# Optimization experiments

Hardware: AMD Instinct MI355X
Metric: run time of the kernel (lower is better)

The kernel has to match this reference:

```python
import jax, jax.numpy as jnp
import numpy as np

IN_C = 128
MID_C = 128
EPS = 1e-5


def layer_norm(x, g, b):
    mu = jnp.mean(x, axis=-1, keepdims=True)
    var = jnp.mean(jnp.square(x - mu), axis=-1, keepdims=True)
    return (x - mu) * jax.lax.rsqrt(var + EPS) * g + b


def setup_inputs() -> dict:
    key = jax.random.key(0)
    ks = jax.random.split(key, 16)
    B, N = 1, 384
    s_in = 1.0 / np.sqrt(IN_C)
    s_mid = 1.0 / np.sqrt(MID_C)
    return {
        "x2d": jax.random.normal(ks[0], (B, N, N, IN_C), dtype=jnp.float32),
        "n1_g": jnp.ones((IN_C,), jnp.float32),
        "n1_b": jnp.zeros((IN_C,), jnp.float32),
        "n2_g": jnp.ones((MID_C,), jnp.float32),
        "n2_b": jnp.zeros((MID_C,), jnp.float32),
        "w1i": jax.random.uniform(ks[1], (MID_C, IN_C), jnp.float32, -s_in, s_in),
        "b1i": jnp.zeros((MID_C,), jnp.float32),
        "w1j": jax.random.uniform(ks[2], (MID_C, IN_C), jnp.float32, -s_in, s_in),
        "b1j": jnp.zeros((MID_C,), jnp.float32),
        "w1i_s": jax.random.uniform(ks[3], (MID_C, IN_C), jnp.float32, -s_in, s_in),
        "b1i_s": jnp.zeros((MID_C,), jnp.float32),
        "w1j_s": jax.random.uniform(ks[4], (MID_C, IN_C), jnp.float32, -s_in, s_in),
        "b1j_s": jnp.zeros((MID_C,), jnp.float32),
        "w2": jax.random.uniform(ks[5], (IN_C, MID_C), jnp.float32, -s_mid, s_mid),
        "b2": jnp.zeros((IN_C,), jnp.float32),
        "w3": jax.random.uniform(ks[6], (IN_C, IN_C), jnp.float32, -s_in, s_in),
        "b3": jnp.zeros((IN_C,), jnp.float32),
    }


def reference(x2d, n1_g, n1_b, n2_g, n2_b, w1i, b1i, w1j, b1j,
              w1i_s, b1i_s, w1j_s, b1j_s, w2, b2, w3, b3):
    # x2d: [B, N, N, C]
    x = layer_norm(x2d, n1_g, n1_b)
    i = (x @ w1i.T + b1i) * jax.nn.sigmoid(x @ w1i_s.T + b1i_s)  # [B,N,N,mid]
    j = (x @ w1j.T + b1j) * jax.nn.sigmoid(x @ w1j_s.T + b1j_s)  # [B,N,N,mid]
    out = jnp.einsum('bikc,bjkc->bijc', i, j)                    # contract over k
    out = layer_norm(out, n2_g, n2_b)
    out = out @ w2.T + b2
    out = out * jax.nn.sigmoid(x @ w3.T + b3)
    return out
```

## Files before the change

### kernel.cpp

```cpp
#include <hip/hip_runtime.h>

#define NN 384
#define CC 128
#define NPOS (NN * NN)

typedef short bf8_t __attribute__((ext_vector_type(8)));
typedef float f32x4_t __attribute__((ext_vector_type(4)));

#define MFMA16(a, b, c) __builtin_amdgcn_mfma_f32_16x16x32_bf16((a), (b), (c), 0, 0, 0)

__device__ __forceinline__ unsigned short f2bf(float f) {
  unsigned int u = __builtin_bit_cast(unsigned int, f);
  u += 0x7fffu + ((u >> 16) & 1u);
  return (unsigned short)(u >> 16);
}
__device__ __forceinline__ float bf2f(unsigned short s) {
  return __builtin_bit_cast(float, ((unsigned int)s) << 16);
}
__device__ __forceinline__ float sigm(float x) { return 1.0f / (1.0f + __expf(-x)); }

__global__ __launch_bounds__(256) void kW(const float* __restrict__ a,
                                          const float* __restrict__ b,
                                          const float* __restrict__ c,
                                          const float* __restrict__ d,
                                          const float* __restrict__ e,
                                          const float* __restrict__ f,
                                          unsigned short* __restrict__ o) {
  int idx = (blockIdx.x * 256 + threadIdx.x) * 4;
  const float* s = f;
  if (idx < 16384) s = a;
  else if (idx < 32768) s = b;
  else if (idx < 49152) s = c;
  else if (idx < 65536) s = d;
  else if (idx < 81920) s = e;
  int off = idx & 16383;
  float4 v = *(const float4*)(s + off);
  o[idx + 0] = f2bf(v.x);
  o[idx + 1] = f2bf(v.y);
  o[idx + 2] = f2bf(v.z);
  o[idx + 3] = f2bf(v.w);
}

__global__ __launch_bounds__(256, 2) void kA(
    const float* __restrict__ x, const float* __restrict__ n1g,
    const float* __restrict__ n1b, const unsigned short* __restrict__ wcat,
    const float* __restrict__ b1i, const float* __restrict__ b1is,
    const float* __restrict__ b1j, const float* __restrict__ b1js,
    const float* __restrict__ b3v, unsigned short* __restrict__ i_s,
    unsigned short* __restrict__ j_s, unsigned short* __restrict__ g3) {
  __shared__ __align__(16) unsigned short lds[17664];
  float* bl = (float*)(lds + 16384);

  int blk = blockIdx.x;
  int ii = blk / 3;
  int k0 = (blk % 3) * 128;
  int t = threadIdx.x;
  int lane = t & 63, wave = t >> 6;
  int lr = lane & 15, lh = lane >> 4;

  if (t < 160) {
    int m = t >> 5, e4 = t & 31;
    const float* bp = (m == 0) ? b1i : (m == 1) ? b1is : (m == 2) ? b1j : (m == 3) ? b1js : b3v;
    ((float4*)bl)[m * 32 + e4] = ((const float4*)bp)[e4];
  }

  {
    int pos = t >> 1, half = t & 1;
    const float* xr = x + (size_t)(ii * NN + k0 + pos) * CC + half * 64;
    float v[64];
    float s = 0.f;
#pragma unroll
    for (int a = 0; a < 16; ++a) {
      float4 f4 = ((const float4*)xr)[a];
      v[4 * a + 0] = f4.x; v[4 * a + 1] = f4.y;
      v[4 * a + 2] = f4.z; v[4 * a + 3] = f4.w;
      s += f4.x + f4.y + f4.z + f4.w;
    }
    s += __shfl_xor(s, 1);
    float mu = s * (1.0f / CC);
    float vs = 0.f;
#pragma unroll
    for (int a = 0; a < 64; ++a) { float d = v[a] - mu; vs += d * d; }
    vs += __shfl_xor(vs, 1);
    float rs = rsqrtf(vs * (1.0f / CC) + 1e-5f);
#pragma unroll
    for (int a8 = 0; a8 < 8; ++a8) {
      union { bf8_t v8; unsigned short e[8]; } u;
#pragma unroll
      for (int e = 0; e < 8; ++e) {
        int c = half * 64 + a8 * 8 + e;
        u.e[e] = f2bf((v[a8 * 8 + e] - mu) * rs * n1g[c] + n1b[c]);
      }
      int slot = (half * 8 + a8) ^ (pos & 7);
      *(bf8_t*)&lds[pos * 128 + slot * 8] = u.v8;
    }
  }
  __syncthreads();

  bf8_t xf[2][4];
#pragma unroll
  for (int nt = 0; nt < 2; ++nt)
#pragma unroll
    for (int kk = 0; kk < 4; ++kk) {
      int row = wave * 32 + nt * 16 + lr;
      int slot = (kk * 4 + lh) ^ (row & 7);
      xf[nt][kk] = *(const bf8_t*)&lds[row * 128 + slot * 8];
    }
  __syncthreads();

  constexpr int blk64[10] = {0, 2, 1, 3, 4, 6, 5, 7, 8, 9};
  auto ISSUE = [&](int k, int bsel) {
    const unsigned short* base = wcat + (size_t)blk64[k] * 8192;
#pragma unroll
    for (int it = 0; it < 4; ++it) {
      int u = it * 256 + t;
      int row = u >> 4, sl = u & 15;
      int slg = sl ^ (row & 7);
      __builtin_amdgcn_global_load_lds(
          (const __attribute__((address_space(1))) unsigned int*)(base + row * CC + slg * 8),
          (__attribute__((address_space(3))) unsigned int*)(lds + bsel * 8192 + u * 8), 16, 0, 0);
    }
  };
  auto COMP = [&](f32x4_t (&A)[4][2], const unsigned short* buf) {
#pragma unroll
    for (int ct = 0; ct < 4; ++ct)
#pragma unroll
      for (int kk = 0; kk < 4; ++kk) {
        int rv = ct * 16 + lr;
        int slot = (kk * 4 + lh) ^ (rv & 7);
        bf8_t w = *(const bf8_t*)&buf[rv * 128 + slot * 8];
#pragma unroll
        for (int nt = 0; nt < 2; ++nt) A[ct][nt] = MFMA16(w, xf[nt][kk], A[ct][nt]);
      }
  };

  f32x4_t z4 = {0.f, 0.f, 0.f, 0.f};
  f32x4_t accV[4][2], accG[4][2], acc3[2][4];
  ISSUE(0, 0);
#pragma unroll 10
  for (int k = 0; k < 10; ++k) {
    if (k == 2 || k == 4 || k == 6 || k == 8 || k == 9)
      asm volatile("s_waitcnt vmcnt(4)" ::: "memory");
    else
      asm volatile("s_waitcnt vmcnt(0)" ::: "memory");
    __builtin_amdgcn_s_barrier();
    __builtin_amdgcn_sched_barrier(0);
    if (k < 9) ISSUE(k + 1, (k + 1) & 1);
    unsigned short* buf = lds + (k & 1) * 8192;
    if (k < 8) {
      if ((k & 1) == 0) {
#pragma unroll
        for (int ct = 0; ct < 4; ++ct)
#pragma unroll
          for (int nt = 0; nt < 2; ++nt) accV[ct][nt] = z4;
        COMP(accV, buf);
      } else {
#pragma unroll
        for (int ct = 0; ct < 4; ++ct)
#pragma unroll
          for (int nt = 0; nt < 2; ++nt) accG[ct][nt] = z4;
        COMP(accG, buf);
        asm volatile("s_waitcnt lgkmcnt(0)" ::: "memory");
        __builtin_amdgcn_s_barrier();
        __builtin_amdgcn_sched_barrier(0);
        int pair = k >> 2, h = (k >> 1) & 1;
#pragma unroll
        for (int ct = 0; ct < 4; ++ct)
#pragma unroll
          for (int nt = 0; nt < 2; ++nt)
#pragma unroll
            for (int r = 0; r < 4; ++r) {
              int cl = ct * 16 + lh * 4 + r;
              int c = h * 64 + cl;
              float val = accV[ct][nt][r] + bl[pair * 256 + c];
              float gat = accG[ct][nt][r] + bl[pair * 256 + 128 + c];
              int pos = wave * 32 + nt * 16 + lr;
              int sw = ((ct * 4 + lh) & 7) << 4;
              buf[cl * 128 + (pos ^ sw)] = f2bf(val * sigm(gat));
            }
        asm volatile("s_waitcnt lgkmcnt(0)" ::: "memory");
        __builtin_amdgcn_s_barrier();
        __builtin_amdgcn_sched_barrier(0);
        unsigned short* dstm = pair ? j_s : i_s;
#pragma unroll
        for (int it = 0; it < 4; ++it) {
          int g = it * 256 + t;
          int cl = g >> 4, ch = g & 15;
          int s = (cl >> 2) & 7;
          bf8_t v = *(const bf8_t*)&buf[cl * 128 + ((ch ^ (s << 1)) * 8)];
          *(bf8_t*)(dstm + ((size_t)(h * 64 + cl) * NN + ii) * NN + k0 + ch * 8) = v;
        }
      }
    } else {
      int h = k - 8;
#pragma unroll
      for (int mt = 0; mt < 2; ++mt)
#pragma unroll
        for (int ct = 0; ct < 4; ++ct) acc3[mt][ct] = z4;
#pragma unroll
      for (int ct = 0; ct < 4; ++ct)
#pragma unroll
        for (int kk = 0; kk < 4; ++kk) {
          int rv = ct * 16 + lr;
          int slot = (kk * 4 + lh) ^ (rv & 7);
          bf8_t w = *(const bf8_t*)&buf[rv * 128 + slot * 8];
#pragma unroll
          for (int mt = 0; mt < 2; ++mt) acc3[mt][ct] = MFMA16(xf[mt][kk], w, acc3[mt][ct]);
        }
      asm volatile("s_waitcnt lgkmcnt(0)" ::: "memory");
      __builtin_amdgcn_s_barrier();
      __builtin_amdgcn_sched_barrier(0);
#pragma unroll
      for (int mt = 0; mt < 2; ++mt)
#pragma unroll
        for (int ct = 0; ct < 4; ++ct)
#pragma unroll
          for (int r = 0; r < 4; ++r) {
            int cl = ct * 16 + lr;
            int pos = wave * 32 + mt * 16 + lh * 4 + r;
            float gv = sigm(acc3[mt][ct][r] + bl[512 + h * 64 + cl]);
            int s2 = (pos >> 2) & 3;
            buf[pos * 64 + (cl ^ (s2 << 4))] = f2bf(gv);
          }
      asm volatile("s_waitcnt lgkmcnt(0)" ::: "memory");
      __builtin_amdgcn_s_barrier();
      __builtin_amdgcn_sched_barrier(0);
#pragma unroll
      for (int it = 0; it < 4; ++it) {
        int g = it * 256 + t;
        int p2 = g >> 3, cc2 = g & 7;
        int s2 = (p2 >> 2) & 3;
        bf8_t v = *(const bf8_t*)&buf[p2 * 64 + ((cc2 ^ (s2 << 1)) * 8)];
        *(bf8_t*)(g3 + (size_t)(ii * NN + k0 + p2) * CC + h * 64 + cc2 * 8) = v;
      }
    }
  }
}

__global__ __launch_bounds__(256) void kB(const unsigned short* __restrict__ i_s,
                                          const unsigned short* __restrict__ j_s,
                                          float* __restrict__ out_pre) {
  __shared__ unsigned short At[128][32];
  __shared__ unsigned short Bt[128][32];
  int b = blockIdx.x;
  int logical = (b & 7) * 144 + (b >> 3);
  int c = logical / 9;
  int tt = logical % 9;
  int i0 = (tt / 3) * 128, j0 = (tt % 3) * 128;
  const unsigned short* Ab = i_s + ((size_t)c * NN + i0) * NN;
  const unsigned short* Bb = j_s + ((size_t)c * NN + j0) * NN;
  int t = threadIdx.x, lane = t & 63, wave = t >> 6;
  int wi = (wave >> 1) * 64, wj = (wave & 1) * 64;
  int lr = lane & 15, lh = lane >> 4;
  int rsub = lane >> 2;
  int ksub = (lane & 3) * 8;

  f32x4_t z4 = {0.f, 0.f, 0.f, 0.f};
  f32x4_t acc[4][4];
#pragma unroll
  for (int mt = 0; mt < 4; ++mt)
#pragma unroll
    for (int nt = 0; nt < 4; ++nt) acc[mt][nt] = z4;

  for (int k0 = 0; k0 < NN; k0 += 32) {
#pragma unroll
    for (int half = 0; half < 2; ++half) {
      int r = half * 64 + wave * 16;
      __builtin_amdgcn_global_load_lds(
          (const __attribute__((address_space(1))) unsigned int*)(Ab + (size_t)(r + rsub) * NN + k0 + ksub),
          (__attribute__((address_space(3))) unsigned int*)&At[r][0], 16, 0, 0);
      __builtin_amdgcn_global_load_lds(
          (const __attribute__((address_space(1))) unsigned int*)(Bb + (size_t)(r + rsub) * NN + k0 + ksub),
          (__attribute__((address_space(3))) unsigned int*)&Bt[r][0], 16, 0, 0);
    }
    __syncthreads();
    bf8_t af2[4], bf2[4];
#pragma unroll
    for (int mt = 0; mt < 4; ++mt) af2[mt] = *(const bf8_t*)&At[wi + mt * 16 + lr][lh * 8];
#pragma unroll
    for (int nt = 0; nt < 4; ++nt) bf2[nt] = *(const bf8_t*)&Bt[wj + nt * 16 + lr][lh * 8];
#pragma unroll
    for (int mt = 0; mt < 4; ++mt)
#pragma unroll
      for (int nt = 0; nt < 4; ++nt) acc[mt][nt] = MFMA16(af2[mt], bf2[nt], acc[mt][nt]);
    __syncthreads();
  }
  float* orow = out_pre + ((size_t)c * NN + (i0 + wi)) * NN + (j0 + wj);
#pragma unroll
  for (int mt = 0; mt < 4; ++mt)
#pragma unroll
    for (int nt = 0; nt < 4; ++nt)
#pragma unroll
      for (int r = 0; r < 4; ++r)
        orow[(size_t)(mt * 16 + lh * 4 + r) * NN + nt * 16 + lr] = acc[mt][nt][r];
}

__global__ __launch_bounds__(256) void kC(const float* __restrict__ out_pre,
                                          const float* __restrict__ n2g,
                                          const float* __restrict__ n2b,
                                          const unsigned short* __restrict__ w2bf,
                                          const float* __restrict__ b2,
                                          const unsigned short* __restrict__ g3,
                                          float* __restrict__ out) {
  __shared__ unsigned short xs2[128][136];
  int b = blockIdx.x;
  int ii = b / 3, j0 = (b % 3) * 128;
  int t = threadIdx.x, lane = t & 63, wave = t >> 6;
  {
    int pos = t >> 1, half = t & 1;
    const float* src = out_pre + (size_t)half * 64 * NPOS + (size_t)ii * NN + j0 + pos;
    float v[64];
    float s = 0.f;
#pragma unroll
    for (int a2 = 0; a2 < 64; ++a2) { v[a2] = src[(size_t)a2 * NPOS]; s += v[a2]; }
    s += __shfl_xor(s, 1);
    float mu = s * (1.0f / CC);
    float vs = 0.f;
#pragma unroll
    for (int a2 = 0; a2 < 64; ++a2) { float d = v[a2] - mu; vs += d * d; }
    vs += __shfl_xor(vs, 1);
    float rs = rsqrtf(vs * (1.0f / CC) + 1e-5f);
#pragma unroll
    for (int a8 = 0; a8 < 8; ++a8) {
      union { bf8_t v8; unsigned short e[8]; } u;
#pragma unroll
      for (int e2 = 0; e2 < 8; ++e2) {
        int c = half * 64 + a8 * 8 + e2;
        u.e[e2] = f2bf((v[a8 * 8 + e2] - mu) * rs * n2g[c] + n2b[c]);
      }
      *(bf8_t*)&xs2[pos][half * 64 + a8 * 8] = u.v8;
    }
  }
  __syncthreads();
  int lr = lane & 15, lh = lane >> 4;
  bf8_t af2[2][4];
#pragma unroll
  for (int mt = 0; mt < 2; ++mt)
#pragma unroll
    for (int kk = 0; kk < 4; ++kk)
      af2[mt][kk] = *(const bf8_t*)&xs2[wave * 32 + mt * 16 + lr][kk * 32 + lh * 8];
  f32x4_t z4 = {0.f, 0.f, 0.f, 0.f};
  f32x4_t acc[2][8];
#pragma unroll
  for (int mt = 0; mt < 2; ++mt)
#pragma unroll
    for (int nt = 0; nt < 8; ++nt) acc[mt][nt] = z4;
#pragma unroll
  for (int nt = 0; nt < 8; ++nt) {
#pragma unroll
    for (int kk = 0; kk < 4; ++kk) {
      bf8_t bw = *(const bf8_t*)(w2bf + (size_t)(nt * 16 + lr) * CC + kk * 32 + lh * 8);
#pragma unroll
      for (int mt = 0; mt < 2; ++mt) acc[mt][nt] = MFMA16(af2[mt][kk], bw, acc[mt][nt]);
    }
  }
#pragma unroll
  for (int mt = 0; mt < 2; ++mt)
#pragma unroll
    for (int nt = 0; nt < 8; ++nt)
#pragma unroll
      for (int r = 0; r < 4; ++r) {
        int posl = wave * 32 + mt * 16 + lh * 4 + r;
        int c = nt * 16 + lr;
        size_t p = (size_t)ii * NN + j0 + posl;
        float y = acc[mt][nt][r] + b2[c];
        out[p * CC + c] = y * bf2f(g3[p * CC + c]);
      }
}

extern "C" void kernel_launch(void* const* d_in, const int* in_sizes, int n_in,
                              void* d_out, int out_size, void* d_ws, size_t ws_size,
                              hipStream_t stream) {
  (void)in_sizes; (void)n_in; (void)out_size; (void)ws_size;
  const float* x2d  = (const float*)d_in[0];
  const float* n1g  = (const float*)d_in[1];
  const float* n1b  = (const float*)d_in[2];
  const float* n2g  = (const float*)d_in[3];
  const float* n2b  = (const float*)d_in[4];
  const float* w1i  = (const float*)d_in[5];
  const float* b1i  = (const float*)d_in[6];
  const float* w1j  = (const float*)d_in[7];
  const float* b1j  = (const float*)d_in[8];
  const float* w1is = (const float*)d_in[9];
  const float* b1is = (const float*)d_in[10];
  const float* w1js = (const float*)d_in[11];
  const float* b1js = (const float*)d_in[12];
  const float* w2   = (const float*)d_in[13];
  const float* b2   = (const float*)d_in[14];
  const float* w3   = (const float*)d_in[15];
  const float* b3   = (const float*)d_in[16];

  char* ws = (char*)d_ws;
  unsigned short* wcat = (unsigned short*)ws;
  size_t TELEMS = (size_t)CC * NN * NN;
  unsigned short* i_s = (unsigned short*)(ws + 262144);
  unsigned short* j_s = i_s + TELEMS;
  unsigned short* g3  = j_s + TELEMS;
  float* out_pre = (float*)(ws + 262144 + 3 * TELEMS * 2);
  float* outp = (float*)d_out;

  kW<<<96, 256, 0, stream>>>(w1i, w1is, w1j, w1js, w3, w2, wcat);
  kA<<<1152, 256, 0, stream>>>(x2d, n1g, n1b, wcat, b1i, b1is, b1j, b1js, b3, i_s, j_s, g3);
  kB<<<1152, 256, 0, stream>>>(i_s, j_s, out_pre);
  kC<<<1152, 256, 0, stream>>>(out_pre, n2g, n2b, wcat + 5 * CC * CC, b2, g3, outp);
}
```

Baseline: 178.7 us.

## Write i/j projections position-major and transpose in a separate kernel

The projection kernel now writes the gated i/j outputs in natural position-major layout. It reuses one epilogue path for both the i/j pairs and the w3 gate. A new kT kernel stages 256-position tiles in LDS and transposes them to channel-major for the triangular contraction kernel. The aim is wider, simpler stores in kA and a single unified epilogue, at the cost of an extra full read and write of both i and j tensors plus a kernel launch. out_pre now aliases the i_nat/j_nat region to save workspace.

```diff
diff --git a/kernel.cpp b/kernel.cpp
--- a/kernel.cpp
+++ b/kernel.cpp
@@ -5,6 +5,7 @@
 #define NPOS (NN * NN)
 
 typedef short bf8_t __attribute__((ext_vector_type(8)));
+typedef short s4_t __attribute__((ext_vector_type(4)));
 typedef float f32x4_t __attribute__((ext_vector_type(4)));
 
 #define MFMA16(a, b, c) __builtin_amdgcn_mfma_f32_16x16x32_bf16((a), (b), (c), 0, 0, 0)
@@ -46,14 +47,15 @@
     const float* __restrict__ n1b, const unsigned short* __restrict__ wcat,
     const float* __restrict__ b1i, const float* __restrict__ b1is,
     const float* __restrict__ b1j, const float* __restrict__ b1js,
-    const float* __restrict__ b3v, unsigned short* __restrict__ i_s,
-    unsigned short* __restrict__ j_s, unsigned short* __restrict__ g3) {
+    const float* __restrict__ b3v, unsigned short* __restrict__ i_nat,
+    unsigned short* __restrict__ j_nat, unsigned short* __restrict__ g3) {
   __shared__ __align__(16) unsigned short lds[17664];
   float* bl = (float*)(lds + 16384);
 
   int blk = blockIdx.x;
   int ii = blk / 3;
   int k0 = (blk % 3) * 128;
+  int p0 = ii * NN + k0;
   int t = threadIdx.x;
   int lane = t & 63, wave = t >> 6;
   int lr = lane & 15, lh = lane >> 4;
@@ -66,7 +68,7 @@
 
   {
     int pos = t >> 1, half = t & 1;
-    const float* xr = x + (size_t)(ii * NN + k0 + pos) * CC + half * 64;
+    const float* xr = x + (size_t)(p0 + pos) * CC + half * 64;
     float v[64];
     float s = 0.f;
 #pragma unroll
@@ -121,7 +123,7 @@
           (__attribute__((address_space(3))) unsigned int*)(lds + bsel * 8192 + u * 8), 16, 0, 0);
     }
   };
-  auto COMP = [&](f32x4_t (&A)[4][2], const unsigned short* buf) {
+  auto COMP = [&](f32x4_t (&A)[2][4], const unsigned short* buf) {
 #pragma unroll
     for (int ct = 0; ct < 4; ++ct)
 #pragma unroll
@@ -130,12 +132,12 @@
         int slot = (kk * 4 + lh) ^ (rv & 7);
         bf8_t w = *(const bf8_t*)&buf[rv * 128 + slot * 8];
 #pragma unroll
-        for (int nt = 0; nt < 2; ++nt) A[ct][nt] = MFMA16(w, xf[nt][kk], A[ct][nt]);
+        for (int nt = 0; nt < 2; ++nt) A[nt][ct] = MFMA16(xf[nt][kk], w, A[nt][ct]);
       }
   };
 
   f32x4_t z4 = {0.f, 0.f, 0.f, 0.f};
-  f32x4_t accV[4][2], accG[4][2], acc3[2][4];
+  f32x4_t accV[2][4], accG[2][4];
   ISSUE(0, 0);
 #pragma unroll 10
   for (int k = 0; k < 10; ++k) {
@@ -147,93 +149,96 @@
     __builtin_amdgcn_sched_barrier(0);
     if (k < 9) ISSUE(k + 1, (k + 1) & 1);
     unsigned short* buf = lds + (k & 1) * 8192;
-    if (k < 8) {
-      if ((k & 1) == 0) {
-#pragma unroll
-        for (int ct = 0; ct < 4; ++ct)
-#pragma unroll
-          for (int nt = 0; nt < 2; ++nt) accV[ct][nt] = z4;
-        COMP(accV, buf);
-      } else {
-#pragma unroll
-        for (int ct = 0; ct < 4; ++ct)
-#pragma unroll
-          for (int nt = 0; nt < 2; ++nt) accG[ct][nt] = z4;
-        COMP(accG, buf);
-        asm volatile("s_waitcnt lgkmcnt(0)" ::: "memory");
-        __builtin_amdgcn_s_barrier();
-        __builtin_amdgcn_sched_barrier(0);
-        int pair = k >> 2, h = (k >> 1) & 1;
-#pragma unroll
-        for (int ct = 0; ct < 4; ++ct)
-#pragma unroll
-          for (int nt = 0; nt < 2; ++nt)
-#pragma unroll
-            for (int r = 0; r < 4; ++r) {
-              int cl = ct * 16 + lh * 4 + r;
-              int c = h * 64 + cl;
-              float val = accV[ct][nt][r] + bl[pair * 256 + c];
-              float gat = accG[ct][nt][r] + bl[pair * 256 + 128 + c];
-              int pos = wave * 32 + nt * 16 + lr;
-              int sw = ((ct * 4 + lh) & 7) << 4;
-              buf[cl * 128 + (pos ^ sw)] = f2bf(val * sigm(gat));
-            }
-        asm volatile("s_waitcnt lgkmcnt(0)" ::: "memory");
-        __builtin_amdgcn_s_barrier();
-        __builtin_amdgcn_sched_barrier(0);
-        unsigned short* dstm = pair ? j_s : i_s;
-#pragma unroll
-        for (int it = 0; it < 4; ++it) {
-          int g = it * 256 + t;
-          int cl = g >> 4, ch = g & 15;
-          int s = (cl >> 2) & 7;
-          bf8_t v = *(const bf8_t*)&buf[cl * 128 + ((ch ^ (s << 1)) * 8)];
-          *(bf8_t*)(dstm + ((size_t)(h * 64 + cl) * NN + ii) * NN + k0 + ch * 8) = v;
-        }
-      }
+    bool isPairV = (k < 8) && ((k & 1) == 0);
+    if (isPairV) {
+#pragma unroll
+      for (int nt = 0; nt < 2; ++nt)
+#pragma unroll
+        for (int ct = 0; ct < 4; ++ct) accV[nt][ct] = z4;
+      COMP(accV, buf);
     } else {
-      int h = k - 8;
-#pragma unroll
-      for (int mt = 0; mt < 2; ++mt)
-#pragma unroll
-        for (int ct = 0; ct < 4; ++ct) acc3[mt][ct] = z4;
-#pragma unroll
-      for (int ct = 0; ct < 4; ++ct)
-#pragma unroll
-        for (int kk = 0; kk < 4; ++kk) {
-          int rv = ct * 16 + lr;
-          int slot = (kk * 4 + lh) ^ (rv & 7);
-          bf8_t w = *(const bf8_t*)&buf[rv * 128 + slot * 8];
-#pragma unroll
-          for (int mt = 0; mt < 2; ++mt) acc3[mt][ct] = MFMA16(xf[mt][kk], w, acc3[mt][ct]);
-        }
+#pragma unroll
+      for (int nt = 0; nt < 2; ++nt)
+#pragma unroll
+        for (int ct = 0; ct < 4; ++ct) accG[nt][ct] = z4;
+      COMP(accG, buf);
       asm volatile("s_waitcnt lgkmcnt(0)" ::: "memory");
       __builtin_amdgcn_s_barrier();
       __builtin_amdgcn_sched_barrier(0);
-#pragma unroll
-      for (int mt = 0; mt < 2; ++mt)
+      int pair = k >> 2;
+      int h = (k < 8) ? ((k >> 1) & 1) : (k - 8);
+      unsigned short* dstm = (k >= 8) ? g3 : (pair ? j_nat : i_nat);
+#pragma unroll
+      for (int nt = 0; nt < 2; ++nt)
 #pragma unroll
         for (int ct = 0; ct < 4; ++ct)
 #pragma unroll
           for (int r = 0; r < 4; ++r) {
+            int pos = wave * 32 + nt * 16 + lh * 4 + r;
             int cl = ct * 16 + lr;
-            int pos = wave * 32 + mt * 16 + lh * 4 + r;
-            float gv = sigm(acc3[mt][ct][r] + bl[512 + h * 64 + cl]);
-            int s2 = (pos >> 2) & 3;
-            buf[pos * 64 + (cl ^ (s2 << 4))] = f2bf(gv);
+            float o;
+            if (k < 8) {
+              float val = accV[nt][ct][r] + bl[pair * 256 + h * 64 + cl];
+              float gat = accG[nt][ct][r] + bl[pair * 256 + 128 + h * 64 + cl];
+              o = val * sigm(gat);
+            } else {
+              o = sigm(accG[nt][ct][r] + bl[512 + h * 64 + cl]);
+            }
+            int slot = (cl >> 3) ^ (pos & 7);
+            buf[pos * 64 + slot * 8 + (cl & 7)] = f2bf(o);
           }
       asm volatile("s_waitcnt lgkmcnt(0)" ::: "memory");
       __builtin_amdgcn_s_barrier();
       __builtin_amdgcn_sched_barrier(0);
 #pragma unroll
       for (int it = 0; it < 4; ++it) {
-        int g = it * 256 + t;
-        int p2 = g >> 3, cc2 = g & 7;
-        int s2 = (p2 >> 2) & 3;
-        bf8_t v = *(const bf8_t*)&buf[p2 * 64 + ((cc2 ^ (s2 << 1)) * 8)];
-        *(bf8_t*)(g3 + (size_t)(ii * NN + k0 + p2) * CC + h * 64 + cc2 * 8) = v;
+        int u = it * 256 + t;
+        int pos = u >> 3, ch = u & 7;
+        int slot = ch ^ (pos & 7);
+        bf8_t v = *(const bf8_t*)&buf[pos * 64 + slot * 8];
+        *(bf8_t*)(dstm + (size_t)(p0 + pos) * CC + h * 64 + ch * 8) = v;
       }
     }
+  }
+}
+
+__global__ __launch_bounds__(256, 2) void kT(const unsigned short* __restrict__ i_nat,
+                                             const unsigned short* __restrict__ j_nat,
+                                             unsigned short* __restrict__ i_T,
+                                             unsigned short* __restrict__ j_T) {
+  __shared__ __align__(16) unsigned short tile[32768];
+  int b = blockIdx.x;
+  const unsigned short* src;
+  unsigned short* dst;
+  int pc;
+  if (b < 576) { pc = b; src = i_nat; dst = i_T; }
+  else         { pc = b - 576; src = j_nat; dst = j_T; }
+  size_t pos0 = (size_t)pc * 256;
+  src += pos0 * CC;
+  int t = threadIdx.x;
+#pragma unroll
+  for (int it = 0; it < 16; ++it) {
+    int u = it * 256 + t;
+    int pos = u >> 4, gr = u & 15;
+    int gsw = gr ^ ((pos >> 2) & 15);
+    __builtin_amdgcn_global_load_lds(
+        (const __attribute__((address_space(1))) unsigned int*)(src + pos * CC + gsw * 8),
+        (__attribute__((address_space(3))) unsigned int*)(tile + u * 8), 16, 0, 0);
+  }
+  asm volatile("s_waitcnt vmcnt(0)" ::: "memory");
+  __syncthreads();
+  int lane = t & 63, w = t >> 6;
+#pragma unroll
+  for (int ci = 0; ci < 32; ++ci) {
+    int c = w * 32 + ci;
+    int sl = ((c >> 3) ^ (lane & 15)) * 8 + (c & 7);
+    int base = lane * 4 * 128;
+    s4_t v;
+    v[0] = (short)tile[base + sl];
+    v[1] = (short)tile[base + 128 + sl];
+    v[2] = (short)tile[base + 256 + sl];
+    v[3] = (short)tile[base + 384 + sl];
+    *(s4_t*)(dst + (size_t)c * NPOS + pos0 + lane * 4) = v;
   }
 }
 
@@ -393,14 +398,17 @@
   char* ws = (char*)d_ws;
   unsigned short* wcat = (unsigned short*)ws;
   size_t TELEMS = (size_t)CC * NN * NN;
-  unsigned short* i_s = (unsigned short*)(ws + 262144);
-  unsigned short* j_s = i_s + TELEMS;
-  unsigned short* g3  = j_s + TELEMS;
-  float* out_pre = (float*)(ws + 262144 + 3 * TELEMS * 2);
+  unsigned short* i_nat = (unsigned short*)(ws + 262144);
+  unsigned short* j_nat = i_nat + TELEMS;
+  unsigned short* g3    = j_nat + TELEMS;
+  unsigned short* i_T   = g3 + TELEMS;
+  unsigned short* j_T   = i_T + TELEMS;
+  float* out_pre = (float*)(ws + 262144);
   float* outp = (float*)d_out;
 
   kW<<<96, 256, 0, stream>>>(w1i, w1is, w1j, w1js, w3, w2, wcat);
-  kA<<<1152, 256, 0, stream>>>(x2d, n1g, n1b, wcat, b1i, b1is, b1j, b1js, b3, i_s, j_s, g3);
-  kB<<<1152, 256, 0, stream>>>(i_s, j_s, out_pre);
+  kA<<<1152, 256, 0, stream>>>(x2d, n1g, n1b, wcat, b1i, b1is, b1j, b1js, b3, i_nat, j_nat, g3);
+  kT<<<1152, 256, 0, stream>>>(i_nat, j_nat, i_T, j_T);
+  kB<<<1152, 256, 0, stream>>>(i_T, j_T, out_pre);
   kC<<<1152, 256, 0, stream>>>(out_pre, n2g, n2b, wcat + 5 * CC * CC, b2, g3, outp);
 }
```

Result: slower. 202.6 us (+13.4%).
